# Performance work log

Measured on AMD Instinct MI355X. Metric: run time of the kernel, lower is better.

## Reference

```python
import jax, jax.numpy as jnp
import numpy as np

B, S, H, DH = 8, 1024, 16, 64
D = H * DH  # d_model = 1024
M_ALPHA = -1e9


def setup_inputs() -> dict:
    key = jax.random.key(0)
    ks = jax.random.split(key, 11)
    scale = 1.0 / np.sqrt(D)
    x = jax.random.normal(ks[0], (B, S, D), dtype=jnp.float32)
    # 0/1 padding mask, shape [B, S, 1] (1 = masked position)
    mask = (jax.random.uniform(ks[1], (B, S, 1)) < 0.25).astype(jnp.float32)
    mk = lambda k: jax.random.normal(k, (D, D), dtype=jnp.float32) * scale
    return {
        "x": x,
        "mask": mask,
        "wq_w": mk(ks[2]), "wq_b": jnp.zeros((D,), jnp.float32),
        "wk_w": mk(ks[3]), "wk_b": jnp.zeros((D,), jnp.float32),
        "wv_w": mk(ks[4]), "wv_b": jnp.zeros((D,), jnp.float32),
        "wo_w": mk(ks[5]), "wo_b": jnp.zeros((D,), jnp.float32),
    }


def _split_heads(t):
    # [B, S, D] -> [B, H, S, DH]
    return t.reshape(B, S, H, DH).transpose(0, 2, 1, 3)


def reference(x, mask, wq_w, wq_b, wk_w, wk_b, wv_w, wv_b, wo_w, wo_b):
    q = _split_heads(x @ wq_w + wq_b)  # [B,H,S,DH]
    k = _split_heads(x @ wk_w + wk_b)
    v = _split_heads(x @ wv_w + wv_b)

    logits = jnp.einsum("bhqd,bhkd->bhqk", q, k) / jnp.sqrt(
        jnp.asarray(DH, jnp.float32))
    qk_values = logits  # pre-mask scaled logits (temperature == 0.0 -> no-op)

    # QK mask path: mask [B,S,1] -> tile to [B,S,S] rows (m[b,i,j] = mask[b,i]),
    # then symmetrize (square) -> mask[b,i] + mask[b,j], clamp at 1.
    m = mask[:, :, 0]                               # [B,S]
    mask_qk = jnp.minimum(1.0, m[:, :, None] + m[:, None, :])  # [B,S,S]
    logits = logits + mask_qk[:, None, :, :] * M_ALPHA

    attn = jax.nn.softmax(logits, axis=-1)          # [B,H,S,S]
    z = jnp.einsum("bhqk,bhkd->bhqd", attn, v)      # [B,H,S,DH]
    z = z.transpose(0, 2, 1, 3).reshape(B, S, D)
    out = z @ wo_w + wo_b
    return (out, attn, qk_values, q, k, v)
```

## Files before the change

### kernel.cpp

```cpp
#include <hip/hip_runtime.h>
#include <hip/hip_bf16.h>
#include <stdint.h>

#define BB 8
#define SS 1024
#define HH 16
#define DHD 64
#define DD 1024

typedef __attribute__((ext_vector_type(8))) short bf16x8;
typedef __attribute__((ext_vector_type(4))) float f32x4;

__device__ __forceinline__ unsigned short f2bf(float f) {
  unsigned u = __builtin_bit_cast(unsigned, f);
  u += 0x7fffu + ((u >> 16) & 1u);
  return (unsigned short)(u >> 16);
}

__device__ __forceinline__ unsigned swz(unsigned a) { return a ^ ((a >> 3) & 0x70u); }

#define GLOAD16(gp, lp)                                                        \
  __builtin_amdgcn_global_load_lds(                                            \
      (const __attribute__((address_space(1))) unsigned int*)(gp),             \
      (__attribute__((address_space(3))) unsigned int*)(lp), 16, 0, 0)

#define MFMA16(a, b, c) __builtin_amdgcn_mfma_f32_16x16x32_bf16(a, b, c, 0, 0, 0)

__global__ __launch_bounds__(256) void cvt_x_kernel(const float* __restrict__ x,
                                                    unsigned short* __restrict__ xb) {
  int i = blockIdx.x * 256 + threadIdx.x;
  float4 v = ((const float4*)x)[i];
  ushort4 o;
  o.x = f2bf(v.x); o.y = f2bf(v.y); o.z = f2bf(v.z); o.w = f2bf(v.w);
  ((ushort4*)xb)[i] = o;
}

__global__ __launch_bounds__(256) void transpose_w_kernel(
    const float* __restrict__ w0, const float* __restrict__ w1,
    const float* __restrict__ w2, const float* __restrict__ w3,
    unsigned short* __restrict__ o0, unsigned short* __restrict__ o1,
    unsigned short* __restrict__ o2, unsigned short* __restrict__ o3) {
  __shared__ float tile[32][33];
  const float* src; unsigned short* dst;
  if (blockIdx.z == 0)      { src = w0; dst = o0; }
  else if (blockIdx.z == 1) { src = w1; dst = o1; }
  else if (blockIdx.z == 2) { src = w2; dst = o2; }
  else                      { src = w3; dst = o3; }
  int n0 = blockIdx.x * 32, k0 = blockIdx.y * 32;
  int tx = threadIdx.x, ty = threadIdx.y;
#pragma unroll
  for (int j = 0; j < 32; j += 8)
    tile[ty + j][tx] = src[(size_t)(k0 + ty + j) * DD + n0 + tx];
  __syncthreads();
#pragma unroll
  for (int j = 0; j < 32; j += 8)
    dst[(size_t)(n0 + ty + j) * DD + k0 + tx] = f2bf(tile[tx][ty + j]);
}

__global__ __launch_bounds__(256) void proj_gemm_kernel(
    const unsigned short* __restrict__ xb,
    const unsigned short* __restrict__ wqt, const unsigned short* __restrict__ wkt,
    const unsigned short* __restrict__ wvt,
    const float* __restrict__ bq, const float* __restrict__ bk, const float* __restrict__ bv,
    float* __restrict__ qo, float* __restrict__ ko, float* __restrict__ vo,
    unsigned short* __restrict__ qb, unsigned short* __restrict__ kbf,
    unsigned short* __restrict__ vt) {
  __shared__ __align__(128) unsigned short smem[2 * 128 * 64];
  unsigned short* As = smem;
  unsigned short* Bs = smem + 128 * 64;
  const int tid = threadIdx.x, lane = tid & 63, w = tid >> 6;
  const int wr = (w >> 1) * 64, wc = (w & 1) * 64;
  const int bid = blockIdx.x;
  const int mblk = (bid & 7) * 8 + (bid >> 3) / 24;
  const int ny = (bid >> 3) % 24;
  const int m0 = mblk * 128;
  const int mat = ny >> 3;
  const int n0 = (ny & 7) * 128;
  const unsigned short* Bg = (mat == 0) ? wqt : (mat == 1) ? wkt : wvt;
  const float* bias = (mat == 0) ? bq : (mat == 1) ? bk : bv;

  f32x4 acc[4][4];
  f32x4 z4 = {0.f, 0.f, 0.f, 0.f};
#pragma unroll
  for (int i = 0; i < 4; ++i)
#pragma unroll
    for (int j = 0; j < 4; ++j) acc[i][j] = z4;

  for (int kt = 0; kt < 1024; kt += 64) {
    __syncthreads();
#pragma unroll
    for (int i = 0; i < 4; ++i) {
      unsigned obase = (unsigned)(w * 4096 + i * 1024);
      unsigned a = swz(obase + (unsigned)lane * 16);
      GLOAD16((const char*)xb + ((size_t)(m0 + (int)(a >> 7)) * 1024 + kt) * 2 + (a & 127),
              (char*)As + obase);
      GLOAD16((const char*)Bg + ((size_t)(n0 + (int)(a >> 7)) * 1024 + kt) * 2 + (a & 127),
              (char*)Bs + obase);
    }
    __syncthreads();
#pragma unroll
    for (int ks = 0; ks < 2; ++ks) {
      bf16x8 af[4], bfr[4];
#pragma unroll
      for (int mi = 0; mi < 4; ++mi) {
        unsigned a = (unsigned)((wr + mi * 16 + (lane & 15)) * 128 + ks * 64 + ((lane >> 4) * 16));
        af[mi] = *(const bf16x8*)((const char*)As + swz(a));
      }
#pragma unroll
      for (int ni = 0; ni < 4; ++ni) {
        unsigned a = (unsigned)((wc + ni * 16 + (lane & 15)) * 128 + ks * 64 + ((lane >> 4) * 16));
        bfr[ni] = *(const bf16x8*)((const char*)Bs + swz(a));
      }
#pragma unroll
      for (int mi = 0; mi < 4; ++mi)
#pragma unroll
        for (int ni = 0; ni < 4; ++ni)
          acc[mi][ni] = MFMA16(af[mi], bfr[ni], acc[mi][ni]);
    }
  }

  float* fo = (mat == 0) ? qo : (mat == 1) ? ko : vo;
  __syncthreads();
  unsigned short* T = smem;

#pragma unroll
  for (int mi = 0; mi < 4; ++mi)
#pragma unroll
    for (int ni = 0; ni < 4; ++ni) {
      int col = n0 + wc + ni * 16 + (lane & 15);
      float bs = bias[col];
#pragma unroll
      for (int r = 0; r < 4; ++r) {
        int row = m0 + wr + mi * 16 + ((lane >> 4) << 2) + r;
        float v = acc[mi][ni][r] + bs;
        int b = row >> 10, s = row & 1023, h = col >> 6, dh = col & 63;
        size_t bh = (size_t)(b * HH + h);
        __builtin_nontemporal_store(v, &fo[(bh * SS + s) * DHD + dh]);
        if (mat == 2) {
          int sl = wr + mi * 16 + ((lane >> 4) << 2) + r;
          int dl = wc + ni * 16 + (lane & 15);
          T[dl * 128 + (sl ^ ((dl & 7) << 4))] = f2bf(v);
        } else if (mat == 0) {
          qb[(bh * SS + s) * DHD + dh] = f2bf(v * 0.125f);
        } else {
          kbf[(bh * SS + s) * DHD + dh] = f2bf(v);
        }
      }
    }

  if (mat == 2) {
    __syncthreads();
    int row = tid >> 1;
    int half = tid & 1;
    int colg = n0 + row;
    int h2 = colg >> 6, dh2 = colg & 63;
    int b = m0 >> 10;
    int sg0 = (m0 & 1023) + half * 64;
    unsigned short* dst = vt + (((size_t)(b * HH + h2)) * DHD + dh2) * SS + sg0;
#pragma unroll
    for (int j = 0; j < 8; ++j) {
      int sc = half * 64 + j * 8;
      bf16x8 vv = *(const bf16x8*)&T[row * 128 + (sc ^ ((row & 7) << 4))];
      *(bf16x8*)(dst + j * 8) = vv;
    }
  }
}

__global__ __launch_bounds__(256) void attn_kernel(
    const unsigned short* __restrict__ qb, const unsigned short* __restrict__ kb,
    const unsigned short* __restrict__ vt, const float* __restrict__ mask,
    float* __restrict__ qk_out, float* __restrict__ attn_out,
    unsigned short* __restrict__ zb) {
  __shared__ __align__(128) unsigned short sbuf[12288];
  __shared__ __align__(16) float mbuf[SS];

  const int tid = threadIdx.x, lane = tid & 63, w = tid >> 6;
  const int fid = blockIdx.x;
  const int s_ = fid >> 3;
  const int qt = s_ & 15;
  const int bh = (fid & 7) + 8 * (s_ >> 4);
  const int b = bh >> 4, h = bh & 15;
  const int r0 = qt * 64 + w * 16;
  const int q15 = lane & 15, G = lane >> 4;

  ((float4*)mbuf)[tid] = ((const float4*)(mask + (size_t)b * SS))[tid];
  __syncthreads();

  bf16x8 aq[2];
  {
    const unsigned short* p = qb + (size_t)bh * SS * DHD + (size_t)(r0 + q15) * DHD + G * 8;
    aq[0] = *(const bf16x8*)p;
    aq[1] = *(const bf16x8*)(p + 32);
  }
  const float mq = mbuf[r0 + q15];

  const unsigned short* kbase = kb + (size_t)bh * SS * DHD;
  const char* vbase = (const char*)(vt + (size_t)bh * DHD * SS);
  float* qrow = qk_out + (size_t)bh * SS * SS + (size_t)(r0 + q15) * SS;
  float* arow = attn_out + (size_t)bh * SS * SS + (size_t)(r0 + q15) * SS;

  float m_run = -INFINITY, l_run = 0.f;

  for (int kt = 0; kt < 8; ++kt) {
    int k0 = kt * 128;
    __syncthreads();
#pragma unroll
    for (int i = 0; i < 4; ++i) {
      unsigned obase = (unsigned)(w * 4096 + i * 1024);
      unsigned a = swz(obase + (unsigned)lane * 16);
      GLOAD16((const char*)(kbase + (size_t)k0 * 64) + a, (char*)sbuf + obase);
    }
    __syncthreads();
    f32x4 sm[8];
#pragma unroll
    for (int ct = 0; ct < 8; ++ct) {
      f32x4 acc = {0.f, 0.f, 0.f, 0.f};
#pragma unroll
      for (int ks = 0; ks < 2; ++ks) {
        unsigned a = (unsigned)((ct * 16 + q15) * 128 + ks * 64 + G * 16);
        bf16x8 bk = *(const bf16x8*)((const char*)sbuf + swz(a));
        acc = MFMA16(bk, aq[ks], acc);
      }
      int c0 = k0 + ct * 16 + G * 4;
      __builtin_nontemporal_store(acc, (f32x4*)(qrow + c0));
      float4 mk4 = *(const float4*)(mbuf + c0);
#pragma unroll
      for (int r = 0; r < 4; ++r) {
        float t = fminf(mq + ((const float*)&mk4)[r], 1.f);
        sm[ct][r] = acc[r] + t * (-1.0e9f);
      }
    }
    float mx = sm[0][0];
#pragma unroll
    for (int ct = 0; ct < 8; ++ct)
#pragma unroll
      for (int r = 0; r < 4; ++r) mx = fmaxf(mx, sm[ct][r]);
    mx = fmaxf(mx, __shfl_xor(mx, 16, 64));
    mx = fmaxf(mx, __shfl_xor(mx, 32, 64));
    float m_new = fmaxf(m_run, mx);
    float es = 0.f;
#pragma unroll
    for (int ct = 0; ct < 8; ++ct)
#pragma unroll
      for (int r = 0; r < 4; ++r) es += __expf(sm[ct][r] - m_new);
    es += __shfl_xor(es, 16, 64);
    es += __shfl_xor(es, 32, 64);
    l_run = l_run * __expf(m_run - m_new) + es;
    m_run = m_new;
  }

  const float inv_l = 1.0f / l_run;

  f32x4 zacc[4];
#pragma unroll
  for (int dt = 0; dt < 4; ++dt) zacc[dt] = (f32x4){0.f, 0.f, 0.f, 0.f};

  unsigned short* kb2 = sbuf;
  unsigned short* vb2 = sbuf + 4096;
  unsigned short* pw  = sbuf + 8192 + w * 1024;
  const unsigned pswz = (unsigned)((q15 & 14) << 3);

  for (int kt = 0; kt < 16; ++kt) {
    int k0 = kt * 64;
    __syncthreads();
#pragma unroll
    for (int i = 0; i < 2; ++i) {
      unsigned obase = (unsigned)(w * 2048 + i * 1024);
      unsigned a = swz(obase + (unsigned)lane * 16);
      GLOAD16((const char*)(kbase + (size_t)k0 * 64) + a, (char*)kb2 + obase);
      GLOAD16(vbase + (size_t)(a >> 7) * (SS * 2) + (size_t)k0 * 2 + (a & 127),
              (char*)vb2 + obase);
    }
    __syncthreads();
#pragma unroll
    for (int ct = 0; ct < 4; ++ct) {
      f32x4 acc = {0.f, 0.f, 0.f, 0.f};
#pragma unroll
      for (int ks = 0; ks < 2; ++ks) {
        unsigned a = (unsigned)((ct * 16 + q15) * 128 + ks * 64 + G * 16);
        bf16x8 bk = *(const bf16x8*)((const char*)kb2 + swz(a));
        acc = MFMA16(bk, aq[ks], acc);
      }
      int c0 = k0 + ct * 16 + G * 4;
      float4 mk4 = *(const float4*)(mbuf + c0);
      f32x4 pn;
#pragma unroll
      for (int r = 0; r < 4; ++r) {
        float t = fminf(mq + ((const float*)&mk4)[r], 1.f);
        pn[r] = __expf(acc[r] + t * (-1.0e9f) - m_run) * inv_l;
      }
      __builtin_nontemporal_store(pn, (f32x4*)(arow + c0));
      unsigned u0 = (unsigned)f2bf(pn[0]) | ((unsigned)f2bf(pn[1]) << 16);
      unsigned u1 = (unsigned)f2bf(pn[2]) | ((unsigned)f2bf(pn[3]) << 16);
      uint2 pkd = {u0, u1};
      *(uint2*)((char*)pw + (((unsigned)(q15 * 128 + ct * 32 + G * 8)) ^ pswz)) = pkd;
    }
    bf16x8 pa[2];
#pragma unroll
    for (int ks = 0; ks < 2; ++ks)
      pa[ks] = *(const bf16x8*)((char*)pw + (((unsigned)(q15 * 128 + ks * 64 + G * 16)) ^ pswz));
#pragma unroll
    for (int dt = 0; dt < 4; ++dt) {
#pragma unroll
      for (int ks = 0; ks < 2; ++ks) {
        unsigned av = (unsigned)((dt * 16 + q15) * 128 + ks * 64 + G * 16);
        bf16x8 bv = *(const bf16x8*)((const char*)vb2 + swz(av));
        zacc[dt] = MFMA16(pa[ks], bv, zacc[dt]);
      }
    }
  }

#pragma unroll
  for (int dt = 0; dt < 4; ++dt)
#pragma unroll
    for (int r = 0; r < 4; ++r) {
      int srow = r0 + G * 4 + r;
      int dcol = dt * 16 + q15;
      zb[((size_t)b * SS + srow) * DD + h * 64 + dcol] = f2bf(zacc[dt][r]);
    }
}

__global__ __launch_bounds__(256) void out_gemm_kernel(
    const unsigned short* __restrict__ zb, const unsigned short* __restrict__ wot,
    const float* __restrict__ bo, float* __restrict__ outp) {
  __shared__ __align__(128) unsigned short As[128 * 64];
  __shared__ __align__(128) unsigned short Bs[128 * 64];
  const int tid = threadIdx.x, lane = tid & 63, w = tid >> 6;
  const int wr = (w >> 1) * 64, wc = (w & 1) * 64;
  const int m0 = blockIdx.x * 128;
  const int n0 = blockIdx.y * 128;

  f32x4 acc[4][4];
  f32x4 z4 = {0.f, 0.f, 0.f, 0.f};
#pragma unroll
  for (int i = 0; i < 4; ++i)
#pragma unroll
    for (int j = 0; j < 4; ++j) acc[i][j] = z4;

  for (int kt = 0; kt < 1024; kt += 64) {
    __syncthreads();
#pragma unroll
    for (int i = 0; i < 4; ++i) {
      unsigned obase = (unsigned)(w * 4096 + i * 1024);
      unsigned a = swz(obase + (unsigned)lane * 16);
      GLOAD16((const char*)zb + ((size_t)(m0 + (int)(a >> 7)) * 1024 + kt) * 2 + (a & 127),
              (char*)As + obase);
      GLOAD16((const char*)wot + ((size_t)(n0 + (int)(a >> 7)) * 1024 + kt) * 2 + (a & 127),
              (char*)Bs + obase);
    }
    __syncthreads();
#pragma unroll
    for (int ks = 0; ks < 2; ++ks) {
      bf16x8 af[4], bfr[4];
#pragma unroll
      for (int mi = 0; mi < 4; ++mi) {
        unsigned a = (unsigned)((wr + mi * 16 + (lane & 15)) * 128 + ks * 64 + ((lane >> 4) * 16));
        af[mi] = *(const bf16x8*)((const char*)As + swz(a));
      }
#pragma unroll
      for (int ni = 0; ni < 4; ++ni) {
        unsigned a = (unsigned)((wc + ni * 16 + (lane & 15)) * 128 + ks * 64 + ((lane >> 4) * 16));
        bfr[ni] = *(const bf16x8*)((const char*)Bs + swz(a));
      }
#pragma unroll
      for (int mi = 0; mi < 4; ++mi)
#pragma unroll
        for (int ni = 0; ni < 4; ++ni)
          acc[mi][ni] = MFMA16(af[mi], bfr[ni], acc[mi][ni]);
    }
  }
#pragma unroll
  for (int mi = 0; mi < 4; ++mi)
#pragma unroll
    for (int ni = 0; ni < 4; ++ni) {
      int col = n0 + wc + ni * 16 + (lane & 15);
      float bs = bo[col];
#pragma unroll
      for (int r = 0; r < 4; ++r) {
        int row = m0 + wr + mi * 16 + ((lane >> 4) << 2) + r;
        __builtin_nontemporal_store(acc[mi][ni][r] + bs, &outp[(size_t)row * DD + col]);
      }
    }
}

extern "C" void kernel_launch(void* const* d_in, const int* in_sizes, int n_in,
                              void* d_out, int out_size, void* d_ws, size_t ws_size,
                              hipStream_t stream) {
  const float* x    = (const float*)d_in[0];
  const float* mask = (const float*)d_in[1];
  const float* wq_w = (const float*)d_in[2];
  const float* wq_b = (const float*)d_in[3];
  const float* wk_w = (const float*)d_in[4];
  const float* wk_b = (const float*)d_in[5];
  const float* wv_w = (const float*)d_in[6];
  const float* wv_b = (const float*)d_in[7];
  const float* wo_w = (const float*)d_in[8];
  const float* wo_b = (const float*)d_in[9];

  float* outp = (float*)d_out;
  float* attn = outp + (size_t)8388608;
  float* qk   = attn + (size_t)134217728;
  float* qo   = qk + (size_t)134217728;
  float* ko   = qo + (size_t)8388608;
  float* vo   = ko + (size_t)8388608;

  char* ws = (char*)d_ws;
  unsigned short* xb  = (unsigned short*)(ws + 0);
  unsigned short* wqt = (unsigned short*)(ws + 16777216);
  unsigned short* wkt = (unsigned short*)(ws + 18874368);
  unsigned short* wvt = (unsigned short*)(ws + 20971520);
  unsigned short* wot = (unsigned short*)(ws + 23068672);
  unsigned short* qb  = (unsigned short*)(ws + 25165824);
  unsigned short* kb  = (unsigned short*)(ws + 41943040);
  unsigned short* vt  = (unsigned short*)(ws + 58720256);
  unsigned short* zb  = (unsigned short*)(ws + 75497472);

  cvt_x_kernel<<<8192, 256, 0, stream>>>(x, xb);
  transpose_w_kernel<<<dim3(32, 32, 4), dim3(32, 8), 0, stream>>>(
      wq_w, wk_w, wv_w, wo_w, wqt, wkt, wvt, wot);
  proj_gemm_kernel<<<1536, 256, 0, stream>>>(
      xb, wqt, wkt, wvt, wq_b, wk_b, wv_b, qo, ko, vo, qb, kb, vt);
  attn_kernel<<<2048, 256, 0, stream>>>(qb, kb, vt, mask, qk, attn, zb);
  out_gemm_kernel<<<dim3(64, 8), 256, 0, stream>>>(zb, wot, wo_b, outp);
}
```

Measured before the change: 499.4 us.

## Split attention into online-softmax flash kernel and separate QK/attn writer kernel

Result: slower. 551.3 us (+10.4%).

```diff
diff --git a/kernel.cpp b/kernel.cpp
--- a/kernel.cpp
+++ b/kernel.cpp
@@ -166,11 +166,10 @@
   }
 }
 
-__global__ __launch_bounds__(256) void attn_kernel(
+__global__ __launch_bounds__(256) void attn_flash_kernel(
     const unsigned short* __restrict__ qb, const unsigned short* __restrict__ kb,
     const unsigned short* __restrict__ vt, const float* __restrict__ mask,
-    float* __restrict__ qk_out, float* __restrict__ attn_out,
-    unsigned short* __restrict__ zb) {
+    float2* __restrict__ ml, unsigned short* __restrict__ zb) {
   __shared__ __align__(128) unsigned short sbuf[12288];
   __shared__ __align__(16) float mbuf[SS];
 
@@ -196,69 +195,16 @@
 
   const unsigned short* kbase = kb + (size_t)bh * SS * DHD;
   const char* vbase = (const char*)(vt + (size_t)bh * DHD * SS);
-  float* qrow = qk_out + (size_t)bh * SS * SS + (size_t)(r0 + q15) * SS;
-  float* arow = attn_out + (size_t)bh * SS * SS + (size_t)(r0 + q15) * SS;
-
-  float m_run = -INFINITY, l_run = 0.f;
-
-  for (int kt = 0; kt < 8; ++kt) {
-    int k0 = kt * 128;
-    __syncthreads();
-#pragma unroll
-    for (int i = 0; i < 4; ++i) {
-      unsigned obase = (unsigned)(w * 4096 + i * 1024);
-      unsigned a = swz(obase + (unsigned)lane * 16);
-      GLOAD16((const char*)(kbase + (size_t)k0 * 64) + a, (char*)sbuf + obase);
-    }
-    __syncthreads();
-    f32x4 sm[8];
-#pragma unroll
-    for (int ct = 0; ct < 8; ++ct) {
-      f32x4 acc = {0.f, 0.f, 0.f, 0.f};
-#pragma unroll
-      for (int ks = 0; ks < 2; ++ks) {
-        unsigned a = (unsigned)((ct * 16 + q15) * 128 + ks * 64 + G * 16);
-        bf16x8 bk = *(const bf16x8*)((const char*)sbuf + swz(a));
-        acc = MFMA16(bk, aq[ks], acc);
-      }
-      int c0 = k0 + ct * 16 + G * 4;
-      __builtin_nontemporal_store(acc, (f32x4*)(qrow + c0));
-      float4 mk4 = *(const float4*)(mbuf + c0);
-#pragma unroll
-      for (int r = 0; r < 4; ++r) {
-        float t = fminf(mq + ((const float*)&mk4)[r], 1.f);
-        sm[ct][r] = acc[r] + t * (-1.0e9f);
-      }
-    }
-    float mx = sm[0][0];
-#pragma unroll
-    for (int ct = 0; ct < 8; ++ct)
-#pragma unroll
-      for (int r = 0; r < 4; ++r) mx = fmaxf(mx, sm[ct][r]);
-    mx = fmaxf(mx, __shfl_xor(mx, 16, 64));
-    mx = fmaxf(mx, __shfl_xor(mx, 32, 64));
-    float m_new = fmaxf(m_run, mx);
-    float es = 0.f;
-#pragma unroll
-    for (int ct = 0; ct < 8; ++ct)
-#pragma unroll
-      for (int r = 0; r < 4; ++r) es += __expf(sm[ct][r] - m_new);
-    es += __shfl_xor(es, 16, 64);
-    es += __shfl_xor(es, 32, 64);
-    l_run = l_run * __expf(m_run - m_new) + es;
-    m_run = m_new;
-  }
-
-  const float inv_l = 1.0f / l_run;
-
-  f32x4 zacc[4];
-#pragma unroll
-  for (int dt = 0; dt < 4; ++dt) zacc[dt] = (f32x4){0.f, 0.f, 0.f, 0.f};
 
   unsigned short* kb2 = sbuf;
   unsigned short* vb2 = sbuf + 4096;
   unsigned short* pw  = sbuf + 8192 + w * 1024;
   const unsigned pswz = (unsigned)((q15 & 14) << 3);
+
+  f32x4 zacc[4];
+#pragma unroll
+  for (int dt = 0; dt < 4; ++dt) zacc[dt] = (f32x4){0.f, 0.f, 0.f, 0.f};
+  float m_run = -INFINITY, l_run = 0.f;
 
   for (int kt = 0; kt < 16; ++kt) {
     int k0 = kt * 64;
@@ -272,6 +218,7 @@
               (char*)vb2 + obase);
     }
     __syncthreads();
+    f32x4 sm[4];
 #pragma unroll
     for (int ct = 0; ct < 4; ++ct) {
       f32x4 acc = {0.f, 0.f, 0.f, 0.f};
@@ -283,18 +230,43 @@
       }
       int c0 = k0 + ct * 16 + G * 4;
       float4 mk4 = *(const float4*)(mbuf + c0);
-      f32x4 pn;
 #pragma unroll
       for (int r = 0; r < 4; ++r) {
         float t = fminf(mq + ((const float*)&mk4)[r], 1.f);
-        pn[r] = __expf(acc[r] + t * (-1.0e9f) - m_run) * inv_l;
-      }
-      __builtin_nontemporal_store(pn, (f32x4*)(arow + c0));
+        sm[ct][r] = acc[r] + t * (-1.0e9f);
+      }
+    }
+    float mx = sm[0][0];
+#pragma unroll
+    for (int ct = 0; ct < 4; ++ct)
+#pragma unroll
+      for (int r = 0; r < 4; ++r) mx = fmaxf(mx, sm[ct][r]);
+    mx = fmaxf(mx, __shfl_xor(mx, 16, 64));
+    mx = fmaxf(mx, __shfl_xor(mx, 32, 64));
+    float m_new = fmaxf(m_run, mx);
+    float scale = __expf(m_run - m_new);
+    float es = 0.f;
+#pragma unroll
+    for (int ct = 0; ct < 4; ++ct) {
+      f32x4 pn;
+#pragma unroll
+      for (int r = 0; r < 4; ++r) { pn[r] = __expf(sm[ct][r] - m_new); es += pn[r]; }
       unsigned u0 = (unsigned)f2bf(pn[0]) | ((unsigned)f2bf(pn[1]) << 16);
       unsigned u1 = (unsigned)f2bf(pn[2]) | ((unsigned)f2bf(pn[3]) << 16);
       uint2 pkd = {u0, u1};
       *(uint2*)((char*)pw + (((unsigned)(q15 * 128 + ct * 32 + G * 8)) ^ pswz)) = pkd;
     }
+    es += __shfl_xor(es, 16, 64);
+    es += __shfl_xor(es, 32, 64);
+    l_run = l_run * scale + es;
+    m_run = m_new;
+    float scr[4];
+#pragma unroll
+    for (int r = 0; r < 4; ++r) scr[r] = __shfl(scale, G * 4 + r, 64);
+#pragma unroll
+    for (int dt = 0; dt < 4; ++dt)
+#pragma unroll
+      for (int r = 0; r < 4; ++r) zacc[dt][r] *= scr[r];
     bf16x8 pa[2];
 #pragma unroll
     for (int ks = 0; ks < 2; ++ks)
@@ -310,14 +282,86 @@
     }
   }
 
+  const float inv_l = 1.0f / l_run;
+  if (G == 0)
+    ml[(size_t)bh * SS + r0 + q15] = make_float2(m_run, inv_l);
+  float invr[4];
+#pragma unroll
+  for (int r = 0; r < 4; ++r) invr[r] = __shfl(inv_l, G * 4 + r, 64);
 #pragma unroll
   for (int dt = 0; dt < 4; ++dt)
 #pragma unroll
     for (int r = 0; r < 4; ++r) {
       int srow = r0 + G * 4 + r;
       int dcol = dt * 16 + q15;
-      zb[((size_t)b * SS + srow) * DD + h * 64 + dcol] = f2bf(zacc[dt][r]);
-    }
+      zb[((size_t)b * SS + srow) * DD + h * 64 + dcol] = f2bf(zacc[dt][r] * invr[r]);
+    }
+}
+
+__global__ __launch_bounds__(256) void qk_attn_writer_kernel(
+    const unsigned short* __restrict__ qb, const unsigned short* __restrict__ kb,
+    const float* __restrict__ mask, const float2* __restrict__ ml,
+    float* __restrict__ qk_out, float* __restrict__ attn_out) {
+  __shared__ __align__(128) unsigned short sbuf[128 * 64];
+  __shared__ __align__(16) float mbuf[SS];
+
+  const int tid = threadIdx.x, lane = tid & 63, w = tid >> 6;
+  const int fid = blockIdx.x;
+  const int s_ = fid >> 3;
+  const int qt = s_ & 15;
+  const int bh = (fid & 7) + 8 * (s_ >> 4);
+  const int b = bh >> 4;
+  const int r0 = qt * 64 + w * 16;
+  const int q15 = lane & 15, G = lane >> 4;
+
+  ((float4*)mbuf)[tid] = ((const float4*)(mask + (size_t)b * SS))[tid];
+  __syncthreads();
+
+  bf16x8 aq[2];
+  {
+    const unsigned short* p = qb + (size_t)bh * SS * DHD + (size_t)(r0 + q15) * DHD + G * 8;
+    aq[0] = *(const bf16x8*)p;
+    aq[1] = *(const bf16x8*)(p + 32);
+  }
+  const float mq = mbuf[r0 + q15];
+  float2 mlv = ml[(size_t)bh * SS + r0 + q15];
+  const float m_fin = mlv.x, inv_l = mlv.y;
+
+  const unsigned short* kbase = kb + (size_t)bh * SS * DHD;
+  float* qrow = qk_out + (size_t)bh * SS * SS + (size_t)(r0 + q15) * SS;
+  float* arow = attn_out + (size_t)bh * SS * SS + (size_t)(r0 + q15) * SS;
+
+  for (int kt = 0; kt < 8; ++kt) {
+    int k0 = kt * 128;
+    __syncthreads();
+#pragma unroll
+    for (int i = 0; i < 4; ++i) {
+      unsigned obase = (unsigned)(w * 4096 + i * 1024);
+      unsigned a = swz(obase + (unsigned)lane * 16);
+      GLOAD16((const char*)(kbase + (size_t)k0 * 64) + a, (char*)sbuf + obase);
+    }
+    __syncthreads();
+#pragma unroll
+    for (int ct = 0; ct < 8; ++ct) {
+      f32x4 acc = {0.f, 0.f, 0.f, 0.f};
+#pragma unroll
+      for (int ks = 0; ks < 2; ++ks) {
+        unsigned a = (unsigned)((ct * 16 + q15) * 128 + ks * 64 + G * 16);
+        bf16x8 bk = *(const bf16x8*)((const char*)sbuf + swz(a));
+        acc = MFMA16(bk, aq[ks], acc);
+      }
+      int c0 = k0 + ct * 16 + G * 4;
+      __builtin_nontemporal_store(acc, (f32x4*)(qrow + c0));
+      float4 mk4 = *(const float4*)(mbuf + c0);
+      f32x4 pn;
+#pragma unroll
+      for (int r = 0; r < 4; ++r) {
+        float t = fminf(mq + ((const float*)&mk4)[r], 1.f);
+        pn[r] = __expf(acc[r] + t * (-1.0e9f) - m_fin) * inv_l;
+      }
+      __builtin_nontemporal_store(pn, (f32x4*)(arow + c0));
+    }
+  }
 }
 
 __global__ __launch_bounds__(256) void out_gemm_kernel(
@@ -414,12 +458,14 @@
   unsigned short* kb  = (unsigned short*)(ws + 41943040);
   unsigned short* vt  = (unsigned short*)(ws + 58720256);
   unsigned short* zb  = (unsigned short*)(ws + 75497472);
+  float2* ml = (float2*)(ws + 0);
 
   cvt_x_kernel<<<8192, 256, 0, stream>>>(x, xb);
   transpose_w_kernel<<<dim3(32, 32, 4), dim3(32, 8), 0, stream>>>(
       wq_w, wk_w, wv_w, wo_w, wqt, wkt, wvt, wot);
   proj_gemm_kernel<<<1536, 256, 0, stream>>>(
       xb, wqt, wkt, wvt, wq_b, wk_b, wv_b, qo, ko, vo, qb, kb, vt);
-  attn_kernel<<<2048, 256, 0, stream>>>(qb, kb, vt, mask, qk, attn, zb);
+  attn_flash_kernel<<<2048, 256, 0, stream>>>(qb, kb, vt, mask, ml, zb);
+  qk_attn_writer_kernel<<<2048, 256, 0, stream>>>(qb, kb, mask, ml, qk, attn);
   out_gemm_kernel<<<dim3(64, 8), 256, 0, stream>>>(zb, wot, wo_b, outp);
 }
```
